# Kernel optimization log

Hardware: AMD Instinct MI355X
Metric: run time of the kernel (lower is better)

Reference implementation:

```python
import jax, jax.numpy as jnp
import numpy as np

B, N, T, E, R, NSEL = 128, 1000, 50, 32000, 4, 500
F0, CF = 3, 20
FS = 2 * CF + F0  # 43


def _conv(x, w, b):
    # NCHW valid conv, stride 1
    y = jax.lax.conv_general_dilated(x, w, (1, 1), 'VALID',
                                     dimension_numbers=('NCHW', 'OIHW', 'NCHW'))
    return y + b[None, :, None, None]


def setup_inputs() -> dict:
    key = jax.random.key(0)
    ks = jax.random.split(key, 20)
    s = 0.1
    return {
        'observation': jax.random.normal(ks[0], (B, F0, N, T), jnp.float32),
        'last_action': jax.random.uniform(ks[1], (B, NSEL + 1), jnp.float32),
        'w_s1': jax.random.normal(ks[2], (3, 3, 1, 3), jnp.float32) * s,
        'b_s1': jax.random.normal(ks[3], (3,), jnp.float32) * s,
        'w_s2': jax.random.normal(ks[4], (20, 3, 1, 48), jnp.float32) * s,
        'b_s2': jax.random.normal(ks[5], (20,), jnp.float32) * s,
        'w_m1': jax.random.normal(ks[6], (3, 3, 1, 21), jnp.float32) * s,
        'b_m1': jax.random.normal(ks[7], (3,), jnp.float32) * s,
        'w_m2': jax.random.normal(ks[8], (20, 3, 1, 30), jnp.float32) * s,
        'b_m2': jax.random.normal(ks[9], (20,), jnp.float32) * s,
        'w_rel': jax.random.normal(ks[10], (R, FS, FS), jnp.float32) * s,
        'w_root': jax.random.normal(ks[11], (FS, FS), jnp.float32) * s,
        'b_g': jax.random.normal(ks[12], (FS,), jnp.float32) * s,
        'w_fin': jax.random.normal(ks[13], (1, 2 * FS + 1, 1, 1), jnp.float32) * s,
        'b_fin': jax.random.normal(ks[14], (1,), jnp.float32) * s,
        'edge_index': jax.random.randint(ks[15], (2, E), 0, N, jnp.int64) if jax.config.jax_enable_x64 else jax.random.randint(ks[15], (2, E), 0, N).astype(jnp.int32),
        'edge_type': jax.random.randint(ks[16], (E,), 0, R).astype(jnp.int32),
        'nodes_to_select': jnp.sort(jax.random.randint(ks[17], (NSEL,), 0, N)).astype(jnp.int32),
    }


def reference(observation, last_action, w_s1, b_s1, w_s2, b_s2, w_m1, b_m1,
              w_m2, b_m2, w_rel, w_root, b_g, w_fin, b_fin,
              edge_index, edge_type, nodes_to_select):
    # temporal feature extraction
    short = jax.nn.relu(_conv(jax.nn.relu(_conv(observation, w_s1, b_s1)), w_s2, b_s2))
    mid = jax.nn.relu(_conv(jax.nn.relu(_conv(observation, w_m1, b_m1)), w_m2, b_m2))
    long = jax.nn.relu(jnp.max(observation, axis=3, keepdims=True))
    temporal = jnp.concatenate([short, mid, long], axis=1)  # [B, 43, N, 1]

    x = temporal[:, :, :, 0].transpose(0, 2, 1)  # [B, N, F]

    # RGCNConv with per-relation mean aggregation
    src, dst = edge_index[0], edge_index[1]
    xw = jnp.einsum('bnf,rfg->bnrg', x, w_rel)        # [B, N, R, F]
    msgs = xw[:, src, edge_type, :]                   # [B, E, F] gather
    seg = dst * R + edge_type                         # per (node, relation) segment
    agg = jax.vmap(lambda m: jax.ops.segment_sum(m, seg, num_segments=N * R))(msgs)
    cnt = jax.ops.segment_sum(jnp.ones((E,), x.dtype), seg, num_segments=N * R)
    inv = jnp.where(cnt > 0, 1.0 / cnt, 0.0)
    agg = (agg * inv[None, :, None]).reshape(B, N, R, FS).sum(axis=2)
    gout = jax.nn.leaky_relu(agg + x @ w_root + b_g, 0.01)  # [B, N, F]

    graph_features = gout.transpose(0, 2, 1)[..., None]     # [B, F, N, 1]
    feat = jnp.concatenate([temporal, graph_features], axis=1)  # [B, 86, N, 1]
    feat = feat[:, :, nodes_to_select, :]                       # [B, 86, NSEL, 1]
    last_stocks = last_action[:, 1:].reshape(B, 1, NSEL, 1)
    feat = jnp.concatenate([last_stocks, feat], axis=1)         # [B, 87, NSEL, 1]

    o = jnp.einsum('bcn,oc->bon', feat[..., 0], w_fin[:, :, 0, 0]) + b_fin[None, :, None]
    o = jnp.concatenate([jnp.zeros((B, 1, 1), o.dtype), o], axis=2)[:, 0, :]  # [B, NSEL+1]
    return jax.nn.softmax(o / 1.0, axis=-1)
```

## Files before the change

kernel.cpp:

```cpp
#include <hip/hip_runtime.h>
#include <hip/hip_fp16.h>
#include <math.h>

#define Bn 128
#define Nn 1000
#define Tn 50
#define En 32000
#define Rn 4
#define FSn 43
#define NSELn 500
#define NFtot (Nn * FSn)

__global__ __launch_bounds__(512) void k_temporal(
    const float* __restrict__ obs,
    const float* __restrict__ w_s1, const float* __restrict__ b_s1,
    const float* __restrict__ w_s2, const float* __restrict__ b_s2,
    const float* __restrict__ w_m1, const float* __restrict__ b_m1,
    const float* __restrict__ w_m2, const float* __restrict__ b_m2,
    float* __restrict__ x)
{
    __shared__ float lds[3 * 64 * 51];

    const int b     = blockIdx.x;
    const int tile0 = blockIdx.y * 64;
    const int tid   = threadIdx.x;
    const int lane  = tid & 63;
    const int w     = __builtin_amdgcn_readfirstlane(tid >> 6);
    const int nrows = (Nn - tile0) < 64 ? (Nn - tile0) : 64;

    for (int c = 0; c < 3; ++c) {
        const float* srcp = obs + ((size_t)(b * 3 + c) * Nn + tile0) * Tn;
        for (int idx = tid; idx < nrows * Tn; idx += 512) {
            const int r = idx / Tn;
            const int t = idx - r * Tn;
            lds[(c * 64 + r) * 51 + t] = srcp[idx];
        }
    }
    __syncthreads();

    float acc[20];
    float mx0 = -1e30f, mx1 = -1e30f, mx2 = -1e30f;

    if (w < 3) {
        #pragma unroll
        for (int o = 0; o < 20; ++o) acc[o] = (w == 0) ? b_s2[o] : 0.f;

        const float s10 = b_s1[0], s11 = b_s1[1], s12 = b_s1[2];
        const int t0 = w * 16;

        #pragma unroll 1
        for (int t = t0; t < t0 + 16; ++t) {
            float ov[9];
            #pragma unroll
            for (int c = 0; c < 3; ++c)
                #pragma unroll
                for (int d = 0; d < 3; ++d)
                    ov[c * 3 + d] = lds[(c * 64 + lane) * 51 + t + d];

            float v0 = s10, v1 = s11, v2 = s12;
            #pragma unroll
            for (int c = 0; c < 3; ++c) {
                v0 += ov[c * 3 + 0] * w_s1[(0 * 3 + c) * 3 + 0]
                    + ov[c * 3 + 1] * w_s1[(0 * 3 + c) * 3 + 1]
                    + ov[c * 3 + 2] * w_s1[(0 * 3 + c) * 3 + 2];
                v1 += ov[c * 3 + 0] * w_s1[(1 * 3 + c) * 3 + 0]
                    + ov[c * 3 + 1] * w_s1[(1 * 3 + c) * 3 + 1]
                    + ov[c * 3 + 2] * w_s1[(1 * 3 + c) * 3 + 2];
                v2 += ov[c * 3 + 0] * w_s1[(2 * 3 + c) * 3 + 0]
                    + ov[c * 3 + 1] * w_s1[(2 * 3 + c) * 3 + 1]
                    + ov[c * 3 + 2] * w_s1[(2 * 3 + c) * 3 + 2];
            }
            v0 = fmaxf(v0, 0.f); v1 = fmaxf(v1, 0.f); v2 = fmaxf(v2, 0.f);
            #pragma unroll
            for (int o = 0; o < 20; ++o) {
                acc[o] += v0 * w_s2[(o * 3 + 0) * 48 + t]
                        + v1 * w_s2[(o * 3 + 1) * 48 + t]
                        + v2 * w_s2[(o * 3 + 2) * 48 + t];
            }
        }

        const int rb0 = (0 * 64 + lane) * 51;
        const int rb1 = (1 * 64 + lane) * 51;
        const int rb2 = (2 * 64 + lane) * 51;
        const int l0 = (w == 0) ? 0 : (w == 1) ? 17 : 34;
        const int l1 = (w == 0) ? 17 : (w == 1) ? 34 : 50;
        #pragma unroll 1
        for (int t = l0; t < l1; ++t) {
            mx0 = fmaxf(mx0, lds[rb0 + t]);
            mx1 = fmaxf(mx1, lds[rb1 + t]);
            mx2 = fmaxf(mx2, lds[rb2 + t]);
        }
    } else {
        #pragma unroll
        for (int o = 0; o < 20; ++o) acc[o] = (w == 3) ? b_m2[o] : 0.f;

        const float m10 = b_m1[0], m11 = b_m1[1], m12 = b_m1[2];
        const int t0 = (w - 3) * 6;

        #pragma unroll 1
        for (int t = t0; t < t0 + 6; ++t) {
            float v0 = m10, v1 = m11, v2 = m12;
            #pragma unroll
            for (int c = 0; c < 3; ++c) {
                const int base = (c * 64 + lane) * 51 + t;
                float p0 = 0.f, p1 = 0.f, p2 = 0.f;
                #pragma unroll
                for (int d = 0; d < 21; ++d) {
                    const float ov = lds[base + d];
                    p0 += ov * w_m1[(0 * 3 + c) * 21 + d];
                    p1 += ov * w_m1[(1 * 3 + c) * 21 + d];
                    p2 += ov * w_m1[(2 * 3 + c) * 21 + d];
                }
                v0 += p0; v1 += p1; v2 += p2;
            }
            v0 = fmaxf(v0, 0.f); v1 = fmaxf(v1, 0.f); v2 = fmaxf(v2, 0.f);
            #pragma unroll
            for (int o = 0; o < 20; ++o) {
                acc[o] += v0 * w_m2[(o * 3 + 0) * 30 + t]
                        + v1 * w_m2[(o * 3 + 1) * 30 + t]
                        + v2 * w_m2[(o * 3 + 2) * 30 + t];
            }
        }
    }

    __syncthreads();
    if (w == 1 || w == 2) {
        float* r = lds + (w - 1) * 1472 + lane;
        #pragma unroll
        for (int o = 0; o < 20; ++o) r[o * 64] = acc[o];
        r[20 * 64] = mx0;
        r[21 * 64] = mx1;
        r[22 * 64] = mx2;
    } else if (w >= 4) {
        float* r = lds + 2944 + (w - 4) * 1280 + lane;
        #pragma unroll
        for (int o = 0; o < 20; ++o) r[o * 64] = acc[o];
    }
    __syncthreads();

    if (lane < nrows) {
        float* xp = x + ((size_t)b * Nn + tile0 + lane) * FSn;
        if (w == 0) {
            #pragma unroll
            for (int o = 0; o < 20; ++o) {
                const int a = o * 64 + lane;
                xp[o] = fmaxf(acc[o] + lds[a] + lds[1472 + a], 0.f);
            }
            {
                const int a0 = 20 * 64 + lane, a1 = 21 * 64 + lane, a2 = 22 * 64 + lane;
                xp[40] = fmaxf(fmaxf(mx0, fmaxf(lds[a0], lds[1472 + a0])), 0.f);
                xp[41] = fmaxf(fmaxf(mx1, fmaxf(lds[a1], lds[1472 + a1])), 0.f);
                xp[42] = fmaxf(fmaxf(mx2, fmaxf(lds[a2], lds[1472 + a2])), 0.f);
            }
        } else if (w == 3) {
            #pragma unroll
            for (int o = 0; o < 20; ++o) {
                const int a = 2944 + o * 64 + lane;
                xp[20 + o] = fmaxf(acc[o] + lds[a] + lds[a + 1280]
                                          + lds[a + 2560] + lds[a + 3840], 0.f);
            }
        }
    }
}

__global__ __launch_bounds__(256) void k_transpose(const float* __restrict__ x,
                                                   __half* __restrict__ xT)
{
    __shared__ float tile[64][129];
    const int c0  = blockIdx.x * 64;
    const int tid = threadIdx.x;

    const int j  = tid & 63;
    const int bs = tid >> 6;
    for (int bb = bs; bb < Bn; bb += 4) {
        int c = c0 + j;
        if (c < NFtot) tile[j][bb] = x[(size_t)bb * NFtot + c];
    }
    __syncthreads();

    const int b  = tid & 127;
    for (int jj = (tid >> 7); jj < 64; jj += 2) {
        int c = c0 + jj;
        if (c < NFtot) xT[(size_t)c * Bn + b] = __float2half(tile[jj][b]);
    }
}

__global__ void k_zero(int* __restrict__ cnt, int* __restrict__ pos)
{
    int i = blockIdx.x * blockDim.x + threadIdx.x;
    if (i < 4096) { cnt[i] = 0; pos[i] = 0; }
}

__global__ void k_count(const int* __restrict__ ei, const int* __restrict__ et,
                        int* __restrict__ cnt)
{
    int e = blockIdx.x * blockDim.x + threadIdx.x;
    if (e < En) {
        int dst = ei[En + e];
        atomicAdd(&cnt[dst * Rn + et[e]], 1);
    }
}

__global__ __launch_bounds__(1024) void k_scan(const int* __restrict__ cnt,
                                               int* __restrict__ off)
{
    __shared__ int sums[1024];
    int tid = threadIdx.x;
    int base = tid * 4;
    int c[4];
    int ts = 0;
    #pragma unroll
    for (int k = 0; k < 4; ++k) {
        int i = base + k;
        c[k] = (i < Nn * Rn) ? cnt[i] : 0;
        ts += c[k];
    }
    sums[tid] = ts;
    __syncthreads();
    for (int d = 1; d < 1024; d <<= 1) {
        int t = 0;
        if (tid >= d) t = sums[tid - d];
        __syncthreads();
        sums[tid] += t;
        __syncthreads();
    }
    int excl = sums[tid] - ts;
    #pragma unroll
    for (int k = 0; k < 4; ++k) {
        int i = base + k;
        off[i] = excl;
        excl += c[k];
    }
}

__global__ void k_fill(const int* __restrict__ ei, const int* __restrict__ et,
                       const int* __restrict__ off, int* __restrict__ pos,
                       int* __restrict__ csr)
{
    int e = blockIdx.x * blockDim.x + threadIdx.x;
    if (e < En) {
        int src = ei[e];
        int dst = ei[En + e];
        int seg = dst * Rn + et[e];
        int p = atomicAdd(&pos[seg], 1);
        csr[off[seg] + p] = src;
    }
}

__global__ __launch_bounds__(256) void k_graph(
    const __half* __restrict__ xT,
    const float* __restrict__ w_rel, const float* __restrict__ w_root,
    const float* __restrict__ b_g,
    const float* __restrict__ w_fin, const float* __restrict__ b_fin,
    const float* __restrict__ la,
    const int* __restrict__ csr, const int* __restrict__ off,
    const int* __restrict__ cnt, const int* __restrict__ sel,
    float* __restrict__ logitT)
{
    __shared__ __align__(16) char smem[22016 + 2048 + 32];
    __half* ab    = (__half*)smem;
    int*    srcs  = (int*)(smem + 22016);
    int*    scnt  = (int*)(smem + 22016 + 2048);
    int*    tcnt  = scnt + 4;
    float*  red   = (float*)smem;

    const int i   = blockIdx.x >> 1;
    const int bh  = blockIdx.x & 1;
    const int dst = sel[i];
    const int tid = threadIdx.x;

    {
        const int r = tid >> 6;
        const int c = cnt[dst * Rn + r];
        const int o = off[dst * Rn + r];
        if ((tid & 63) == 0) { tcnt[r] = c; scnt[r] = (c < 128) ? c : 128; }
        #pragma unroll
        for (int j = (tid & 63); j < 128; j += 64)
            if (j < c) srcs[r * 128 + j] = csr[o + j];
    }
    __syncthreads();

    {
        const int r  = tid >> 6;
        const int fc = (tid >> 4) & 3;
        const int b2 = tid & 15;
        const int nk = (fc < 3) ? 11 : 10;

        float4 acc[11];
        #pragma unroll
        for (int k = 0; k < 11; ++k) acc[k] = make_float4(0.f, 0.f, 0.f, 0.f);

        const int cc = scnt[r];
        const float2* xT2 = (const float2*)xT;
        for (int j = 0; j < cc; ++j) {
            const int src = srcs[r * 128 + j];
            const float2* base = xT2 + (size_t)src * (FSn * 32)
                               + (size_t)fc * 32 + bh * 16 + b2;
            #pragma unroll
            for (int k = 0; k < 11; ++k) {
                if (k < nk) {
                    float2 raw = base[(size_t)k * 128];
                    const __half2 h0 = ((const __half2*)&raw)[0];
                    const __half2 h1 = ((const __half2*)&raw)[1];
                    const float2 f0 = __half22float2(h0);
                    const float2 f1 = __half22float2(h1);
                    acc[k].x += f0.x; acc[k].y += f0.y;
                    acc[k].z += f1.x; acc[k].w += f1.y;
                }
            }
        }

        const int  tc  = tcnt[r];
        const float inv = (tc > 0) ? 1.f / (float)tc : 0.f;
        float2* ab2 = (float2*)ab;
        #pragma unroll
        for (int k = 0; k < 11; ++k) {
            if (k < nk) {
                const int f = fc + 4 * k;
                float2 st;
                ((__half2*)&st)[0] = __floats2half2_rn(acc[k].x * inv, acc[k].y * inv);
                ((__half2*)&st)[1] = __floats2half2_rn(acc[k].z * inv, acc[k].w * inv);
                ab2[(r * FSn + f) * 16 + b2] = st;
            }
        }
    }
    __syncthreads();

    const int fs = tid >> 6;
    const int bL = tid & 63;
    const int b  = bh * 64 + bL;
    const int f0 = fs * 11;
    const int nf = (fs == 3) ? 10 : 11;

    float a[5][11];
    #pragma unroll
    for (int rr = 0; rr < 4; ++rr) {
        #pragma unroll
        for (int k = 0; k < 11; ++k)
            a[rr][k] = (k < nf) ? __half2float(ab[(rr * FSn + f0 + k) * 64 + bL]) : 0.f;
    }
    {
        const __half* xp = xT + ((size_t)dst * FSn + f0) * Bn + b;
        #pragma unroll
        for (int k = 0; k < 11; ++k)
            a[4][k] = (k < nf) ? __half2float(xp[(size_t)k * Bn]) : 0.f;
    }

    float accg[FSn];
    #pragma unroll
    for (int g = 0; g < FSn; ++g) accg[g] = 0.f;
    float psum = 0.f;

    #pragma unroll
    for (int k = 0; k < 11; ++k) {
        if (k < nf) {
            const int f = f0 + k;
            #pragma unroll
            for (int rr = 0; rr < 5; ++rr) {
                const float av = a[rr][k];
                const float* wrow = (rr < 4)
                    ? (w_rel + ((size_t)rr * FSn + f) * FSn)
                    : (w_root + (size_t)f * FSn);
                #pragma unroll
                for (int g = 0; g < FSn; ++g) accg[g] += av * wrow[g];
            }
            psum += a[4][k] * w_fin[1 + f];
        }
    }

    __syncthreads();

    if (fs == 3) {
        #pragma unroll
        for (int g = 0; g < FSn; ++g) red[g * 64 + bL] = accg[g];
        red[FSn * 64 + bL] = psum;
    }
    __syncthreads();
    if (fs == 2) {
        #pragma unroll
        for (int g = 0; g < FSn; ++g) red[g * 64 + bL] += accg[g];
        red[FSn * 64 + bL] += psum;
    }
    __syncthreads();
    if (fs == 1) {
        #pragma unroll
        for (int g = 0; g < FSn; ++g) red[g * 64 + bL] += accg[g];
        red[FSn * 64 + bL] += psum;
    }
    __syncthreads();
    if (fs == 0) {
        float logit = b_fin[0] + w_fin[0] * la[(size_t)b * (NSELn + 1) + 1 + i]
                    + psum + red[FSn * 64 + bL];
        #pragma unroll
        for (int g = 0; g < FSn; ++g) {
            float v = accg[g] + red[g * 64 + bL] + b_g[g];
            v = (v > 0.f) ? v : 0.01f * v;
            logit += v * w_fin[44 + g];
        }
        logitT[(size_t)i * Bn + b] = logit;
    }
}

__global__ __launch_bounds__(512) void k_softmax(const float* __restrict__ logitT,
                                                 float* __restrict__ out)
{
    __shared__ float red[512];
    const int b   = blockIdx.x;
    const int tid = threadIdx.x;

    const float l = (tid < NSELn) ? logitT[(size_t)tid * Bn + b] : -1e30f;
    red[tid] = l;
    __syncthreads();
    for (int s = 256; s > 0; s >>= 1) {
        if (tid < s) red[tid] = fmaxf(red[tid], red[tid + s]);
        __syncthreads();
    }
    const float m = fmaxf(red[0], 0.f);
    __syncthreads();

    const float e = (tid < NSELn) ? expf(l - m) : 0.f;
    red[tid] = e;
    __syncthreads();
    for (int s = 256; s > 0; s >>= 1) {
        if (tid < s) red[tid] += red[tid + s];
        __syncthreads();
    }
    const float e0  = expf(-m);
    const float inv = 1.f / (red[0] + e0);

    if (tid == 0) out[(size_t)b * (NSELn + 1)] = e0 * inv;
    if (tid < NSELn) out[(size_t)b * (NSELn + 1) + 1 + tid] = e * inv;
}

extern "C" void kernel_launch(void* const* d_in, const int* in_sizes, int n_in,
                              void* d_out, int out_size, void* d_ws, size_t ws_size,
                              hipStream_t stream)
{
    const float* obs    = (const float*)d_in[0];
    const float* la     = (const float*)d_in[1];
    const float* w_s1   = (const float*)d_in[2];
    const float* b_s1   = (const float*)d_in[3];
    const float* w_s2   = (const float*)d_in[4];
    const float* b_s2   = (const float*)d_in[5];
    const float* w_m1   = (const float*)d_in[6];
    const float* b_m1   = (const float*)d_in[7];
    const float* w_m2   = (const float*)d_in[8];
    const float* b_m2   = (const float*)d_in[9];
    const float* w_rel  = (const float*)d_in[10];
    const float* w_root = (const float*)d_in[11];
    const float* b_g    = (const float*)d_in[12];
    const float* w_fin  = (const float*)d_in[13];
    const float* b_fin  = (const float*)d_in[14];
    const int*   ei     = (const int*)d_in[15];
    const int*   et     = (const int*)d_in[16];
    const int*   sel    = (const int*)d_in[17];
    float*       out    = (float*)d_out;

    char* wsb     = (char*)d_ws;
    float* x      = (float*)wsb;
    __half* xTh   = (__half*)(wsb + 22016000);
    int*   cnt    = (int*)(wsb + 33024000);
    int*   offb   = cnt + 4096;
    int*   pos    = offb + 4096;
    int*   csr    = pos + 4096;
    float* logitT = (float*)(csr + 32000);

    hipLaunchKernelGGL(k_zero,  dim3(16),  dim3(256), 0, stream, cnt, pos);
    hipLaunchKernelGGL(k_count, dim3((En + 255) / 256), dim3(256), 0, stream, ei, et, cnt);
    hipLaunchKernelGGL(k_scan,  dim3(1),   dim3(1024), 0, stream, cnt, offb);
    hipLaunchKernelGGL(k_fill,  dim3((En + 255) / 256), dim3(256), 0, stream, ei, et, offb, pos, csr);

    hipLaunchKernelGGL(k_temporal, dim3(Bn, (Nn + 63) / 64), dim3(512), 0, stream,
                       obs, w_s1, b_s1, w_s2, b_s2, w_m1, b_m1, w_m2, b_m2, x);

    hipLaunchKernelGGL(k_transpose, dim3((NFtot + 63) / 64), dim3(256), 0, stream, x, xTh);

    hipLaunchKernelGGL(k_graph, dim3(NSELn * 2), dim3(256), 0, stream,
                       xTh, w_rel, w_root, b_g, w_fin, b_fin, la,
                       csr, offb, cnt, sel, logitT);

    hipLaunchKernelGGL(k_softmax, dim3(Bn), dim3(512), 0, stream, logitT, out);
}
```

Baseline: 228.3 us.

## Restructure temporal conv into two-stage LDS pipeline with fp16 intermediates

The temporal kernel is rebuilt. It first computes the first-layer conv outputs for all time steps into shared memory as fp16, then runs the second-layer reduction as a separate phase split across warps by output channel. This replaces the fused per-timestep accumulation and the cross-warp partial-sum merge. The observation tile is staged in LDS as fp16, and the intermediate x buffer is written coalesced as fp16, which halves global traffic for x and for the transpose kernel. Converting observations and intermediates to fp16 adds rounding error, and the occupancy hint may raise register pressure.

Measured after the change: 356.4 us. 1.56x slower.

```diff
diff --git a/kernel.cpp b/kernel.cpp
--- a/kernel.cpp
+++ b/kernel.cpp
@@ -11,15 +11,18 @@
 #define NSELn 500
 #define NFtot (Nn * FSn)
 
-__global__ __launch_bounds__(512) void k_temporal(
+__global__ __launch_bounds__(512, 4) void k_temporal(
     const float* __restrict__ obs,
     const float* __restrict__ w_s1, const float* __restrict__ b_s1,
     const float* __restrict__ w_s2, const float* __restrict__ b_s2,
     const float* __restrict__ w_m1, const float* __restrict__ b_m1,
     const float* __restrict__ w_m2, const float* __restrict__ b_m2,
-    float* __restrict__ x)
-{
-    __shared__ float lds[3 * 64 * 51];
+    __half* __restrict__ x)
+{
+    __shared__ __half obs_h[3 * 64 * 52];
+    __shared__ __half y1h[64 * 246];
+    __shared__ float  longp[2 * 3 * 64];
+    __shared__ __half xout[64 * 44];
 
     const int b     = blockIdx.x;
     const int tile0 = blockIdx.y * 64;
@@ -33,140 +36,171 @@
         for (int idx = tid; idx < nrows * Tn; idx += 512) {
             const int r = idx / Tn;
             const int t = idx - r * Tn;
-            lds[(c * 64 + r) * 51 + t] = srcp[idx];
-        }
-    }
-    __syncthreads();
-
-    float acc[20];
-    float mx0 = -1e30f, mx1 = -1e30f, mx2 = -1e30f;
-
-    if (w < 3) {
-        #pragma unroll
-        for (int o = 0; o < 20; ++o) acc[o] = (w == 0) ? b_s2[o] : 0.f;
-
+            obs_h[(c * 64 + r) * 52 + t] = __float2half(srcp[idx]);
+        }
+    }
+    __syncthreads();
+
+    if (w < 2) {
         const float s10 = b_s1[0], s11 = b_s1[1], s12 = b_s1[2];
-        const int t0 = w * 16;
+        const int t0  = w * 24;
+        const int rb0 = lane * 52 + t0;
+        const int rb1 = 64 * 52 + rb0;
+        const int rb2 = 2 * 64 * 52 + rb0;
+
+        float a0 = __half2float(obs_h[rb0]), p0 = __half2float(obs_h[rb0 + 1]);
+        float a1 = __half2float(obs_h[rb1]), p1 = __half2float(obs_h[rb1 + 1]);
+        float a2 = __half2float(obs_h[rb2]), p2 = __half2float(obs_h[rb2 + 1]);
+
+        #pragma unroll 4
+        for (int t = 0; t < 24; ++t) {
+            const float c0 = __half2float(obs_h[rb0 + t + 2]);
+            const float c1 = __half2float(obs_h[rb1 + t + 2]);
+            const float c2 = __half2float(obs_h[rb2 + t + 2]);
+            float v0 = s10 + a0 * w_s1[0]  + p0 * w_s1[1]  + c0 * w_s1[2]
+                           + a1 * w_s1[3]  + p1 * w_s1[4]  + c1 * w_s1[5]
+                           + a2 * w_s1[6]  + p2 * w_s1[7]  + c2 * w_s1[8];
+            float v1 = s11 + a0 * w_s1[9]  + p0 * w_s1[10] + c0 * w_s1[11]
+                           + a1 * w_s1[12] + p1 * w_s1[13] + c1 * w_s1[14]
+                           + a2 * w_s1[15] + p2 * w_s1[16] + c2 * w_s1[17];
+            float v2 = s12 + a0 * w_s1[18] + p0 * w_s1[19] + c0 * w_s1[20]
+                           + a1 * w_s1[21] + p1 * w_s1[22] + c1 * w_s1[23]
+                           + a2 * w_s1[24] + p2 * w_s1[25] + c2 * w_s1[26];
+            const int tt = t0 + t;
+            y1h[lane * 246 +  0 + tt] = __float2half(fmaxf(v0, 0.f));
+            y1h[lane * 246 + 48 + tt] = __float2half(fmaxf(v1, 0.f));
+            y1h[lane * 246 + 96 + tt] = __float2half(fmaxf(v2, 0.f));
+            a0 = p0; p0 = c0; a1 = p1; p1 = c1; a2 = p2; p2 = c2;
+        }
+
+        const int l0 = w * 25;
+        float mx0 = -1e30f, mx1 = -1e30f, mx2 = -1e30f;
+        const int q0 = lane * 52;
+        #pragma unroll 5
+        for (int t = l0; t < l0 + 25; ++t) {
+            mx0 = fmaxf(mx0, __half2float(obs_h[q0 + t]));
+            mx1 = fmaxf(mx1, __half2float(obs_h[64 * 52 + q0 + t]));
+            mx2 = fmaxf(mx2, __half2float(obs_h[2 * 64 * 52 + q0 + t]));
+        }
+        longp[(w * 3 + 0) * 64 + lane] = mx0;
+        longp[(w * 3 + 1) * 64 + lane] = mx1;
+        longp[(w * 3 + 2) * 64 + lane] = mx2;
+    } else {
+        const int idx2 = w - 2;
+        const int i    = idx2 >> 1;
+        const int th   = idx2 & 1;
+        const int t0   = th * 15;
+        const float* wm = w_m1 + i * 63;
+        const float bi  = b_m1[i];
+
+        float y[15];
+        #pragma unroll
+        for (int t = 0; t < 15; ++t) y[t] = bi;
+
+        const int ra = lane * 52 + t0;
+        #pragma unroll
+        for (int tau = 0; tau < 35; ++tau) {
+            const float o0 = __half2float(obs_h[ra + tau]);
+            const float o1 = __half2float(obs_h[64 * 52 + ra + tau]);
+            const float o2 = __half2float(obs_h[2 * 64 * 52 + ra + tau]);
+            const int tlo = (tau - 20 < 0) ? 0 : tau - 20;
+            const int thi = (tau < 14) ? tau : 14;
+            #pragma unroll
+            for (int t = tlo; t <= thi; ++t) {
+                const int d = tau - t;
+                y[t] += o0 * wm[d] + o1 * wm[21 + d] + o2 * wm[42 + d];
+            }
+        }
+        #pragma unroll
+        for (int t = 0; t < 15; ++t)
+            y1h[lane * 246 + 144 + i * 30 + t0 + t] = __float2half(fmaxf(y[t], 0.f));
+    }
+    __syncthreads();
+
+    if (w < 4) {
+        const int ob = w * 5;
+        float acc[5];
+        #pragma unroll
+        for (int q = 0; q < 5; ++q) acc[q] = b_s2[ob + q];
 
         #pragma unroll 1
-        for (int t = t0; t < t0 + 16; ++t) {
-            float ov[9];
+        for (int c = 0; c < 3; ++c) {
+            float yv[48];
+            const int yb = lane * 246 + c * 48;
+            #pragma unroll 8
+            for (int t = 0; t < 48; ++t) yv[t] = __half2float(y1h[yb + t]);
             #pragma unroll
-            for (int c = 0; c < 3; ++c)
+            for (int q = 0; q < 5; ++q) {
+                const float* wr = w_s2 + ((ob + q) * 3 + c) * 48;
+                float s0 = 0.f, s1 = 0.f, s2 = 0.f, s3 = 0.f;
                 #pragma unroll
-                for (int d = 0; d < 3; ++d)
-                    ov[c * 3 + d] = lds[(c * 64 + lane) * 51 + t + d];
-
-            float v0 = s10, v1 = s11, v2 = s12;
+                for (int t = 0; t < 48; t += 4) {
+                    s0 += yv[t]     * wr[t];
+                    s1 += yv[t + 1] * wr[t + 1];
+                    s2 += yv[t + 2] * wr[t + 2];
+                    s3 += yv[t + 3] * wr[t + 3];
+                }
+                acc[q] += (s0 + s1) + (s2 + s3);
+            }
+        }
+        #pragma unroll
+        for (int q = 0; q < 5; ++q)
+            xout[lane * 44 + ob + q] = __float2half(fmaxf(acc[q], 0.f));
+    } else {
+        const int ob = 20 + (w - 4) * 5;
+        float acc[5];
+        #pragma unroll
+        for (int q = 0; q < 5; ++q) acc[q] = b_m2[ob - 20 + q];
+
+        #pragma unroll 1
+        for (int c = 0; c < 3; ++c) {
+            float yv[30];
+            const int yb = lane * 246 + 144 + c * 30;
+            #pragma unroll 6
+            for (int t = 0; t < 30; ++t) yv[t] = __half2float(y1h[yb + t]);
             #pragma unroll
-            for (int c = 0; c < 3; ++c) {
-                v0 += ov[c * 3 + 0] * w_s1[(0 * 3 + c) * 3 + 0]
-                    + ov[c * 3 + 1] * w_s1[(0 * 3 + c) * 3 + 1]
-                    + ov[c * 3 + 2] * w_s1[(0 * 3 + c) * 3 + 2];
-                v1 += ov[c * 3 + 0] * w_s1[(1 * 3 + c) * 3 + 0]
-                    + ov[c * 3 + 1] * w_s1[(1 * 3 + c) * 3 + 1]
-                    + ov[c * 3 + 2] * w_s1[(1 * 3 + c) * 3 + 2];
-                v2 += ov[c * 3 + 0] * w_s1[(2 * 3 + c) * 3 + 0]
-                    + ov[c * 3 + 1] * w_s1[(2 * 3 + c) * 3 + 1]
-                    + ov[c * 3 + 2] * w_s1[(2 * 3 + c) * 3 + 2];
-            }
-            v0 = fmaxf(v0, 0.f); v1 = fmaxf(v1, 0.f); v2 = fmaxf(v2, 0.f);
+            for (int q = 0; q < 5; ++q) {
+                const float* wr = w_m2 + ((ob - 20 + q) * 3 + c) * 30;
+                float s0 = 0.f, s1 = 0.f, s2 = 0.f;
+                #pragma unroll
+                for (int t = 0; t < 30; t += 3) {
+                    s0 += yv[t]     * wr[t];
+                    s1 += yv[t + 1] * wr[t + 1];
+                    s2 += yv[t + 2] * wr[t + 2];
+                }
+                acc[q] += s0 + s1 + s2;
+            }
+        }
+        #pragma unroll
+        for (int q = 0; q < 5; ++q)
+            xout[lane * 44 + ob + q] = __float2half(fmaxf(acc[q], 0.f));
+
+        if (w == 4) {
             #pragma unroll
-            for (int o = 0; o < 20; ++o) {
-                acc[o] += v0 * w_s2[(o * 3 + 0) * 48 + t]
-                        + v1 * w_s2[(o * 3 + 1) * 48 + t]
-                        + v2 * w_s2[(o * 3 + 2) * 48 + t];
-            }
-        }
-
-        const int rb0 = (0 * 64 + lane) * 51;
-        const int rb1 = (1 * 64 + lane) * 51;
-        const int rb2 = (2 * 64 + lane) * 51;
-        const int l0 = (w == 0) ? 0 : (w == 1) ? 17 : 34;
-        const int l1 = (w == 0) ? 17 : (w == 1) ? 34 : 50;
-        #pragma unroll 1
-        for (int t = l0; t < l1; ++t) {
-            mx0 = fmaxf(mx0, lds[rb0 + t]);
-            mx1 = fmaxf(mx1, lds[rb1 + t]);
-            mx2 = fmaxf(mx2, lds[rb2 + t]);
-        }
-    } else {
-        #pragma unroll
-        for (int o = 0; o < 20; ++o) acc[o] = (w == 3) ? b_m2[o] : 0.f;
-
-        const float m10 = b_m1[0], m11 = b_m1[1], m12 = b_m1[2];
-        const int t0 = (w - 3) * 6;
-
-        #pragma unroll 1
-        for (int t = t0; t < t0 + 6; ++t) {
-            float v0 = m10, v1 = m11, v2 = m12;
-            #pragma unroll
-            for (int c = 0; c < 3; ++c) {
-                const int base = (c * 64 + lane) * 51 + t;
-                float p0 = 0.f, p1 = 0.f, p2 = 0.f;
-                #pragma unroll
-                for (int d = 0; d < 21; ++d) {
-                    const float ov = lds[base + d];
-                    p0 += ov * w_m1[(0 * 3 + c) * 21 + d];
-                    p1 += ov * w_m1[(1 * 3 + c) * 21 + d];
-                    p2 += ov * w_m1[(2 * 3 + c) * 21 + d];
-                }
-                v0 += p0; v1 += p1; v2 += p2;
-            }
-            v0 = fmaxf(v0, 0.f); v1 = fmaxf(v1, 0.f); v2 = fmaxf(v2, 0.f);
-            #pragma unroll
-            for (int o = 0; o < 20; ++o) {
-                acc[o] += v0 * w_m2[(o * 3 + 0) * 30 + t]
-                        + v1 * w_m2[(o * 3 + 1) * 30 + t]
-                        + v2 * w_m2[(o * 3 + 2) * 30 + t];
-            }
-        }
-    }
-
-    __syncthreads();
-    if (w == 1 || w == 2) {
-        float* r = lds + (w - 1) * 1472 + lane;
-        #pragma unroll
-        for (int o = 0; o < 20; ++o) r[o * 64] = acc[o];
-        r[20 * 64] = mx0;
-        r[21 * 64] = mx1;
-        r[22 * 64] = mx2;
-    } else if (w >= 4) {
-        float* r = lds + 2944 + (w - 4) * 1280 + lane;
-        #pragma unroll
-        for (int o = 0; o < 20; ++o) r[o * 64] = acc[o];
-    }
-    __syncthreads();
-
-    if (lane < nrows) {
-        float* xp = x + ((size_t)b * Nn + tile0 + lane) * FSn;
-        if (w == 0) {
-            #pragma unroll
-            for (int o = 0; o < 20; ++o) {
-                const int a = o * 64 + lane;
-                xp[o] = fmaxf(acc[o] + lds[a] + lds[1472 + a], 0.f);
-            }
-            {
-                const int a0 = 20 * 64 + lane, a1 = 21 * 64 + lane, a2 = 22 * 64 + lane;
-                xp[40] = fmaxf(fmaxf(mx0, fmaxf(lds[a0], lds[1472 + a0])), 0.f);
-                xp[41] = fmaxf(fmaxf(mx1, fmaxf(lds[a1], lds[1472 + a1])), 0.f);
-                xp[42] = fmaxf(fmaxf(mx2, fmaxf(lds[a2], lds[1472 + a2])), 0.f);
-            }
-        } else if (w == 3) {
-            #pragma unroll
-            for (int o = 0; o < 20; ++o) {
-                const int a = 2944 + o * 64 + lane;
-                xp[20 + o] = fmaxf(acc[o] + lds[a] + lds[a + 1280]
-                                          + lds[a + 2560] + lds[a + 3840], 0.f);
-            }
-        }
-    }
-}
-
-__global__ __launch_bounds__(256) void k_transpose(const float* __restrict__ x,
+            for (int cc = 0; cc < 3; ++cc) {
+                const float m = fmaxf(longp[(0 * 3 + cc) * 64 + lane],
+                                      longp[(1 * 3 + cc) * 64 + lane]);
+                xout[lane * 44 + 40 + cc] = __float2half(fmaxf(m, 0.f));
+            }
+        }
+    }
+    __syncthreads();
+
+    {
+        __half* xp = x + ((size_t)b * Nn + tile0) * FSn;
+        const int total = nrows * FSn;
+        for (int idx = tid; idx < total; idx += 512) {
+            const int nn = idx / FSn;
+            const int f  = idx - nn * FSn;
+            xp[idx] = xout[nn * 44 + f];
+        }
+    }
+}
+
+__global__ __launch_bounds__(256) void k_transpose(const __half* __restrict__ x,
                                                    __half* __restrict__ xT)
 {
-    __shared__ float tile[64][129];
+    __shared__ __half tile[64][132];
     const int c0  = blockIdx.x * 64;
     const int tid = threadIdx.x;
 
@@ -181,7 +215,7 @@
     const int b  = tid & 127;
     for (int jj = (tid >> 7); jj < 64; jj += 2) {
         int c = c0 + jj;
-        if (c < NFtot) xT[(size_t)c * Bn + b] = __float2half(tile[jj][b]);
+        if (c < NFtot) xT[(size_t)c * Bn + b] = tile[jj][b];
     }
 }
 
@@ -457,9 +491,9 @@
     float*       out    = (float*)d_out;
 
     char* wsb     = (char*)d_ws;
-    float* x      = (float*)wsb;
-    __half* xTh   = (__half*)(wsb + 22016000);
-    int*   cnt    = (int*)(wsb + 33024000);
+    __half* x     = (__half*)wsb;
+    __half* xTh   = (__half*)(wsb + 11008000);
+    int*   cnt    = (int*)(wsb + 22016000);
     int*   offb   = cnt + 4096;
     int*   pos    = offb + 4096;
     int*   csr    = pos + 4096;
```
